# Kernel optimization log

Hardware: AMD Instinct MI355X
Metric: run time of the kernel (lower is better)

Reference implementation:

```python
import jax, jax.numpy as jnp
import numpy as np

NEG_SLOPE = 0.2

def _l2norm(x):
    # F.normalize(x, 2, -1): x / max(||x||_2, 1e-12)
    return x / jnp.maximum(jnp.linalg.norm(x, axis=-1, keepdims=True), 1e-12)

def _segment_softmax(e, dst, n_dst):
    m = jax.ops.segment_max(e, dst, num_segments=n_dst)
    m = jnp.where(jnp.isfinite(m), m, 0.0)
    ex = jnp.exp(e - m[dst])
    denom = jax.ops.segment_sum(ex, dst, num_segments=n_dst)
    return ex / (denom[dst] + 1e-16)

def _gat_conv(x_src, x_dst, edge_index, W, a_src, a_dst, b, n_dst):
    # PyG GATConv, heads=1, concat, shared lin for src/dst (int in_channels)
    h_src = x_src @ W                      # [Ns, H]
    h_dst = x_dst @ W                      # [Nd, H]
    src, dst = edge_index[0], edge_index[1]
    al_s = h_src @ a_src                   # [Ns]
    al_d = h_dst @ a_dst                   # [Nd]
    e = jax.nn.leaky_relu(al_s[src] + al_d[dst], NEG_SLOPE)  # [E]
    coef = _segment_softmax(e, dst, n_dst)                   # [E]
    out = jax.ops.segment_sum(coef[:, None] * h_src[src], dst, num_segments=n_dst)
    return out + b

def setup_inputs() -> dict:
    key = jax.random.key(0)
    ks = jax.random.split(key, 32)
    nd, npr, nc, H, L, B = 2000, 19000, 100, 256, 2, 8192
    E_pp, E_dp, E_cp = 400000, 60000, 300000
    s = 0.1
    inp = {
        'drug_emb': jax.random.normal(ks[0], (nd, H), jnp.float32),
        'protein_emb': jax.random.normal(ks[1], (npr, H), jnp.float32),
        'cell_emb': jax.random.normal(ks[2], (nc, H), jnp.float32),
        'W_pp': jax.random.normal(ks[3], (L, H, H), jnp.float32) * s,
        'as_pp': jax.random.normal(ks[4], (L, H), jnp.float32) * s,
        'ad_pp': jax.random.normal(ks[5], (L, H), jnp.float32) * s,
        'b_pp': jax.random.normal(ks[6], (L, H), jnp.float32) * s,
        'W_dp': jax.random.normal(ks[7], (L, H, H), jnp.float32) * s,
        'as_dp': jax.random.normal(ks[8], (L, H), jnp.float32) * s,
        'ad_dp': jax.random.normal(ks[9], (L, H), jnp.float32) * s,
        'b_dp': jax.random.normal(ks[10], (L, H), jnp.float32) * s,
        'W_cp': jax.random.normal(ks[11], (L, H, H), jnp.float32) * s,
        'as_cp': jax.random.normal(ks[12], (L, H), jnp.float32) * s,
        'ad_cp': jax.random.normal(ks[13], (L, H), jnp.float32) * s,
        'b_cp': jax.random.normal(ks[14], (L, H), jnp.float32) * s,
        'W1': jax.random.normal(ks[15], (3 * H, 6 * H), jnp.float32) * s,
        'b1': jax.random.normal(ks[16], (6 * H,), jnp.float32) * s,
        'W2': jax.random.normal(ks[17], (6 * H, 2 * H), jnp.float32) * s,
        'b2': jax.random.normal(ks[18], (2 * H,), jnp.float32) * s,
        'W3': jax.random.normal(ks[19], (2 * H, 2), jnp.float32) * s,
        'b3': jax.random.normal(ks[20], (2,), jnp.float32) * s,
        'edge_pp': jnp.stack([jax.random.randint(ks[21], (E_pp,), 0, npr),
                              jax.random.randint(ks[22], (E_pp,), 0, npr)]),
        'edge_dp': jnp.stack([jax.random.randint(ks[23], (E_dp,), 0, npr),
                              jax.random.randint(ks[24], (E_dp,), 0, nd)]),
        'edge_cp': jnp.stack([jax.random.randint(ks[25], (E_cp,), 0, npr),
                              jax.random.randint(ks[26], (E_cp,), 0, nc)]),
        'drug1': jax.random.randint(ks[27], (B,), 0, nd),
        'drug2': jax.random.randint(ks[28], (B,), 0, nd),
        'cell': jax.random.randint(ks[29], (B,), 0, nc),
    }
    return inp

def reference(drug_emb, protein_emb, cell_emb,
              W_pp, as_pp, ad_pp, b_pp,
              W_dp, as_dp, ad_dp, b_dp,
              W_cp, as_cp, ad_cp, b_cp,
              W1, b1, W2, b2, W3, b3,
              edge_pp, edge_dp, edge_cp, drug1, drug2, cell):
    n_drug, n_prot, n_cell = drug_emb.shape[0], protein_emb.shape[0], cell_emb.shape[0]
    num_layer = W_pp.shape[0]
    # node ids are arange -> embedding lookup is the full table
    x_d, x_p, x_c = drug_emb, protein_emb, cell_emb
    # p-p GATConv adds self loops (default add_self_loops=True)
    loop = jnp.arange(n_prot, dtype=edge_pp.dtype)
    ei_pp = jnp.concatenate([edge_pp, jnp.stack([loop, loop])], axis=1)
    for l in range(num_layer):
        x_p = _gat_conv(x_p, x_p, ei_pp, W_pp[l], as_pp[l], ad_pp[l], b_pp[l], n_prot)
        x_p = _l2norm(x_p)
        x_d = jax.nn.relu(_gat_conv(x_p, x_d, edge_dp, W_dp[l], as_dp[l], ad_dp[l], b_dp[l], n_drug))
        x_c = jax.nn.relu(_gat_conv(x_p, x_c, edge_cp, W_cp[l], as_cp[l], ad_cp[l], b_cp[l], n_cell))
    hid = jnp.concatenate([_l2norm(x_d[drug1]), _l2norm(x_d[drug2]), _l2norm(x_c[cell])], axis=1)
    h = jax.nn.relu(hid @ W1 + b1)
    h = jax.nn.relu(h @ W2 + b2)
    logits = h @ W3 + b3
    return logits
```

## Files before the change

kernel.cpp:

```cpp
#include <hip/hip_runtime.h>
#include <hip/hip_bf16.h>

#define HDIM 256
#define NEG_SLOPE 0.2f
#define NB 128
#define SLICES 8
#define TBN 64
#define TBK 32

typedef __attribute__((ext_vector_type(8))) short bf16x8;
typedef __attribute__((ext_vector_type(4))) float f32x4;

__device__ inline uint f2pl(float x) {
  __hip_bfloat16 h = __float2bfloat16(x);
  ushort hi = *(ushort*)&h;
  float r = x - __bfloat162float(h);
  __hip_bfloat16 l = __float2bfloat16(r);
  ushort lo = *(ushort*)&l;
  return (uint)hi | ((uint)lo << 16);
}
__device__ inline ushort f2b(float x) {
  __hip_bfloat16 h = __float2bfloat16(x);
  return *(ushort*)&h;
}
__device__ inline float b2f(ushort u) {
  uint x = ((uint)u) << 16;
  return __int_as_float((int)x);
}

static inline int cdiv(int a, int b) { return (a + b - 1) / b; }

__global__ void fillf_kernel(float* __restrict__ p, float v, int n) {
  int i = blockIdx.x * blockDim.x + threadIdx.x;
  if (i < n) p[i] = v;
}

__global__ void fill_out2_kernel(float* __restrict__ out, const float* __restrict__ b3, int M) {
  int i = blockIdx.x * 256 + threadIdx.x;
  if (i >= M) return;
  out[(size_t)i * 2 + 0] = b3[0];
  out[(size_t)i * 2 + 1] = b3[1];
}

__global__ void wconv_split_kernel(const float* __restrict__ W,
                                   ushort* __restrict__ WTh, ushort* __restrict__ WTl,
                                   int K, int N) {
  int i = blockIdx.x * 256 + threadIdx.x;
  if (i >= K * N) return;
  int k = i / N, n = i - k * N;
  uint p = f2pl(W[i]);
  WTh[(size_t)n * K + k] = (ushort)(p & 0xffff);
  WTl[(size_t)n * K + k] = (ushort)(p >> 16);
}

__global__ void wconv_split3_kernel(
    const float* __restrict__ Wpp, const float* __restrict__ Wdp, const float* __restrict__ Wcp,
    ushort* __restrict__ WTpph, ushort* __restrict__ WTppl,
    ushort* __restrict__ WTdph, ushort* __restrict__ WTdpl,
    ushort* __restrict__ WTcph, ushort* __restrict__ WTcpl, int L) {
  const int per = HDIM * HDIM;
  int i = blockIdx.x * 256 + threadIdx.x;
  if (i >= 3 * L * per) return;
  int mat = i / per;
  int r = i - mat * per;
  int l = mat / 3, ty = mat - l * 3;
  const float* W = (ty == 0 ? Wpp : ty == 1 ? Wdp : Wcp) + (size_t)l * per;
  ushort* Th = (ty == 0 ? WTpph : ty == 1 ? WTdph : WTcph) + (size_t)l * per;
  ushort* Tl = (ty == 0 ? WTppl : ty == 1 ? WTdpl : WTcpl) + (size_t)l * per;
  int k = r >> 8, n = r & (HDIM - 1);
  uint p = f2pl(W[r]);
  Th[(size_t)n * HDIM + k] = (ushort)(p & 0xffff);
  Tl[(size_t)n * HDIM + k] = (ushort)(p >> 16);
}

__global__ void f32_to_split_kernel(const float* __restrict__ in,
                                    ushort* __restrict__ oh, ushort* __restrict__ ol, int n) {
  int i = blockIdx.x * 256 + threadIdx.x;
  if (i >= n) return;
  uint p = f2pl(in[i]);
  oh[i] = (ushort)(p & 0xffff);
  ol[i] = (ushort)(p >> 16);
}

__global__ __launch_bounds__(256) void matvec_all_kernel(
    const float* __restrict__ Wpp, const float* __restrict__ aspp, const float* __restrict__ adpp,
    const float* __restrict__ Wdp, const float* __restrict__ asdp, const float* __restrict__ addp,
    const float* __restrict__ Wcp, const float* __restrict__ ascp, const float* __restrict__ adcp,
    float* __restrict__ wv) {
  int b = blockIdx.x;
  int l = b / 6, r = b - l * 6, type = r >> 1, isd = r & 1;
  const float* W = (type == 0 ? Wpp : type == 1 ? Wdp : Wcp) + (size_t)l * HDIM * HDIM;
  const float* a = (type == 0 ? (isd ? adpp : aspp)
                  : type == 1 ? (isd ? addp : asdp)
                              : (isd ? adcp : ascp)) + (size_t)l * HDIM;
  int k = threadIdx.x;
  const float4* Wr = (const float4*)(W + (size_t)k * HDIM);
  float s = 0.f;
#pragma unroll 8
  for (int n4 = 0; n4 < HDIM / 4; ++n4) {
    float4 w = Wr[n4];
    float4 av = *(const float4*)(a + n4 * 4);
    s += w.x * av.x + w.y * av.y + w.z * av.z + w.w * av.w;
  }
  wv[(size_t)b * HDIM + k] = s;
}

__global__ __launch_bounds__(256) void prep_p_kernel(
    const float* __restrict__ in, ushort* __restrict__ outb,
    const float* __restrict__ a1, const float* __restrict__ a2,
    float* __restrict__ o1, float* __restrict__ o2, int n) {
  int row = blockIdx.x * 4 + (threadIdx.x >> 6);
  if (row >= n) return;
  int lane = threadIdx.x & 63;
  float s1 = 0.f, s2 = 0.f;
#pragma unroll
  for (int u = 0; u < 4; ++u) {
    int c = lane + u * 64;
    float hv = in[(size_t)row * HDIM + c];
    outb[(size_t)row * HDIM + c] = f2b(hv);
    s1 += hv * a1[c];
    s2 += hv * a2[c];
  }
#pragma unroll
  for (int off = 32; off; off >>= 1) {
    s1 += __shfl_down(s1, off);
    s2 += __shfl_down(s2, off);
  }
  if (lane == 0) { o1[row] = s1; o2[row] = s2; }
}

__global__ __launch_bounds__(256) void combine_h1_kernel(
    const float* __restrict__ P1, const float* __restrict__ P2, const float* __restrict__ P3,
    const int* __restrict__ g1, const int* __restrict__ g2, const int* __restrict__ g3,
    int row0, ushort* __restrict__ h1h, ushort* __restrict__ h1l, int M, int K) {
  int t = blockIdx.x * 256 + threadIdx.x;
  int kq = K >> 2;
  if (t >= M * kq) return;
  int row = t / kq, c4 = t - row * kq;
  int bi = row0 + row;
  size_t o = (size_t)c4 * 4;
  float4 a = *(const float4*)(P1 + (size_t)g1[bi] * K + o);
  float4 b = *(const float4*)(P2 + (size_t)g2[bi] * K + o);
  float4 c = *(const float4*)(P3 + (size_t)g3[bi] * K + o);
  uint p0 = f2pl(fmaxf(a.x + b.x + c.x, 0.f));
  uint p1 = f2pl(fmaxf(a.y + b.y + c.y, 0.f));
  uint p2 = f2pl(fmaxf(a.z + b.z + c.z, 0.f));
  uint p3 = f2pl(fmaxf(a.w + b.w + c.w, 0.f));
  ushort4 h = {(ushort)(p0 & 0xffff), (ushort)(p1 & 0xffff), (ushort)(p2 & 0xffff), (ushort)(p3 & 0xffff)};
  ushort4 l = {(ushort)(p0 >> 16), (ushort)(p1 >> 16), (ushort)(p2 >> 16), (ushort)(p3 >> 16)};
  *(ushort4*)(h1h + (size_t)row * K + o) = h;
  *(ushort4*)(h1l + (size_t)row * K + o) = l;
}

template <int TBM_, int ACT, int FUSE3>
__global__ __launch_bounds__(256) void mfma_gemm(
    const ushort* __restrict__ Ahg, const ushort* __restrict__ Alg,
    const ushort* __restrict__ Bhg, const ushort* __restrict__ Blg,
    int ldb, const float* __restrict__ bias, const float* __restrict__ W3g,
    float* __restrict__ C, int M, int N, int K) {
  __shared__ __align__(16) ushort Ah[2][4][TBM_ / 16][16][8];
  __shared__ __align__(16) ushort Al[2][4][TBM_ / 16][16][8];
  __shared__ __align__(16) ushort Bh[2][4][TBN / 16][16][8];
  __shared__ __align__(16) ushort Bl[2][4][TBN / 16][16][8];

  constexpr int NU = TBM_ / 64;
  constexpr int TM = TBM_ / 32;

  const int tid = threadIdx.x;
  const int lane = tid & 63;
  const int wid = tid >> 6;
  const int wm = wid & 1, wn = wid >> 1;
  const int l16 = lane & 15;
  const int quad = lane >> 4;
  const int m0 = blockIdx.x * TBM_;
  const int n0 = blockIdx.y * TBN;

  const int gq = lane & 3;
  const int co = gq * 8;
  const int r4 = lane >> 2;
  const int wslot = (r4 + 2 * gq) & 15;
  const int rslot = (l16 + 2 * quad) & 15;

  uint4 rah0[NU], ral0[NU], rbh0, rbl0;
  uint4 rah1[NU], ral1[NU], rbh1, rbl1;

  auto LOADA = [&](uint4* rah, uint4* ral, uint4& rbh, uint4& rbl, int k0) {
#pragma unroll
    for (int u = 0; u < NU; ++u) {
      int r = wid * (TBM_ / 4) + r4 + 16 * u;
      int gm = m0 + r;
      if (gm < M) {
        size_t o = (size_t)gm * K + k0 + co;
        rah[u] = *(const uint4*)(Ahg + o);
        ral[u] = *(const uint4*)(Alg + o);
      } else {
        rah[u] = make_uint4(0, 0, 0, 0);
        ral[u] = make_uint4(0, 0, 0, 0);
      }
    }
    {
      int r = wid * 16 + r4;
      size_t o = (size_t)(n0 + r) * ldb + k0 + co;
      rbh = *(const uint4*)(Bhg + o);
      rbl = *(const uint4*)(Blg + o);
    }
  };
  auto STORE = [&](const uint4* rah, const uint4* ral, const uint4& rbh, const uint4& rbl, int b) {
#pragma unroll
    for (int u = 0; u < NU; ++u) {
      int ch = (wid * (TBM_ / 4) + 16 * u) >> 4;
      *(uint4*)&Ah[b][gq][ch][wslot][0] = rah[u];
      *(uint4*)&Al[b][gq][ch][wslot][0] = ral[u];
    }
    *(uint4*)&Bh[b][gq][wid][wslot][0] = rbh;
    *(uint4*)&Bl[b][gq][wid][wslot][0] = rbl;
  };

  f32x4 acc[TM][2];
#pragma unroll
  for (int i = 0; i < TM; ++i)
#pragma unroll
    for (int j = 0; j < 2; ++j) acc[i][j] = (f32x4){0.f, 0.f, 0.f, 0.f};

  auto COMPUTE = [&](int b) {
    bf16x8 ahf[TM], alf[TM], bhf[2], blf[2];
#pragma unroll
    for (int t = 0; t < TM; ++t) {
      int ch = wm * (TBM_ / 32) + t;
      ahf[t] = *(const bf16x8*)&Ah[b][quad][ch][rslot][0];
      alf[t] = *(const bf16x8*)&Al[b][quad][ch][rslot][0];
    }
#pragma unroll
    for (int t = 0; t < 2; ++t) {
      int ch = wn * 2 + t;
      bhf[t] = *(const bf16x8*)&Bh[b][quad][ch][rslot][0];
      blf[t] = *(const bf16x8*)&Bl[b][quad][ch][rslot][0];
    }
#pragma unroll
    for (int tm = 0; tm < TM; ++tm)
#pragma unroll
      for (int tn = 0; tn < 2; ++tn) {
        acc[tm][tn] = __builtin_amdgcn_mfma_f32_16x16x32_bf16(ahf[tm], bhf[tn], acc[tm][tn], 0, 0, 0);
        acc[tm][tn] = __builtin_amdgcn_mfma_f32_16x16x32_bf16(ahf[tm], blf[tn], acc[tm][tn], 0, 0, 0);
        acc[tm][tn] = __builtin_amdgcn_mfma_f32_16x16x32_bf16(alf[tm], bhf[tn], acc[tm][tn], 0, 0, 0);
      }
  };

  const int NK = K / TBK;
  LOADA(rah0, ral0, rbh0, rbl0, 0);
  LOADA(rah1, ral1, rbh1, rbl1, TBK);
  STORE(rah0, ral0, rbh0, rbl0, 0);
  int k = 2 * TBK;
  for (int t = 0; t < (NK - 2) / 2; ++t) {
    __syncthreads();
    LOADA(rah0, ral0, rbh0, rbl0, k);
    COMPUTE(0);
    STORE(rah1, ral1, rbh1, rbl1, 1);
    k += TBK;
    __syncthreads();
    LOADA(rah1, ral1, rbh1, rbl1, k);
    COMPUTE(1);
    STORE(rah0, ral0, rbh0, rbl0, 0);
    k += TBK;
  }
  __syncthreads();
  COMPUTE(0);
  STORE(rah1, ral1, rbh1, rbl1, 1);
  __syncthreads();
  COMPUTE(1);

  if (FUSE3) {
#pragma unroll
    for (int tm = 0; tm < TM; ++tm) {
#pragma unroll
      for (int r = 0; r < 4; ++r) {
        int row = m0 + wm * (TBM_ / 2) + tm * 16 + quad * 4 + r;
        float s0 = 0.f, s1 = 0.f;
#pragma unroll
        for (int tn = 0; tn < 2; ++tn) {
          int col = n0 + wn * 32 + tn * 16 + l16;
          float v = fmaxf(acc[tm][tn][r] + bias[col], 0.f);
          s0 += v * W3g[col * 2 + 0];
          s1 += v * W3g[col * 2 + 1];
        }
#pragma unroll
        for (int o = 1; o < 16; o <<= 1) {
          s0 += __shfl_xor(s0, o);
          s1 += __shfl_xor(s1, o);
        }
        if (l16 == 0 && row < M) {
          atomicAdd(&C[(size_t)row * 2 + 0], s0);
          atomicAdd(&C[(size_t)row * 2 + 1], s1);
        }
      }
    }
  } else {
#pragma unroll
    for (int tn = 0; tn < 2; ++tn) {
      int col = n0 + wn * 32 + tn * 16 + l16;
      float bv = bias ? bias[col] : 0.f;
#pragma unroll
      for (int tm = 0; tm < TM; ++tm) {
#pragma unroll
        for (int r = 0; r < 4; ++r) {
          int row = m0 + wm * (TBM_ / 2) + tm * 16 + quad * 4 + r;
          if (row >= M) continue;
          float v = acc[tm][tn][r] + bv;
          if (ACT == 1) v = fmaxf(v, 0.f);
          C[(size_t)row * N + col] = v;
        }
      }
    }
  }
}

template <int TBM_, int ACT>
static void gemm_launch(hipStream_t s,
                        const ushort* Ahg, const ushort* Alg,
                        const ushort* Bhg, const ushort* Blg,
                        int ldb, const float* bias, float* C,
                        int M, int N, int K) {
  dim3 g(cdiv(M, TBM_), N / TBN);
  mfma_gemm<TBM_, ACT, 0><<<g, 256, 0, s>>>(Ahg, Alg, Bhg, Blg, ldb, bias, nullptr, C, M, N, K);
}

static void gemm_launch_f3(hipStream_t s,
                           const ushort* Ahg, const ushort* Alg,
                           const ushort* Bhg, const ushort* Blg,
                           int ldb, const float* bias, const float* W3,
                           float* C, int M, int N, int K) {
  dim3 g(cdiv(M, 64), N / TBN);
  mfma_gemm<64, 1, 1><<<g, 256, 0, s>>>(Ahg, Alg, Bhg, Blg, ldb, bias, W3, C, M, N, K);
}

__global__ __launch_bounds__(256) void rowdot_kernel(
    const float* __restrict__ H, const float* __restrict__ a,
    float* __restrict__ out, int n) {
  int row = blockIdx.x * 4 + (threadIdx.x >> 6);
  if (row >= n) return;
  int lane = threadIdx.x & 63;
  const float* h = H + (size_t)row * HDIM;
  float s = 0.f;
#pragma unroll
  for (int u = 0; u < 4; ++u) {
    int c = lane + u * 64;
    s += h[c] * a[c];
  }
#pragma unroll
  for (int off = 32; off; off >>= 1) s += __shfl_down(s, off);
  if (lane == 0) out[row] = s;
}

__global__ __launch_bounds__(256) void hist_kernel(
    const int* __restrict__ src, const int* __restrict__ dst, int E, int nloops,
    int Nd, int* __restrict__ offs) {
  extern __shared__ int bins[];
  int tot = E + nloops;
  int chunk = (tot + NB - 1) / NB;
  int b = blockIdx.x;
  int s0 = b * chunk, s1 = min(s0 + chunk, tot);
  for (int i = threadIdx.x; i < Nd; i += 256) bins[i] = 0;
  __syncthreads();
  for (int i = s0 + threadIdx.x; i < s1; i += 256) {
    int d = (i < E) ? dst[i] : (i - E);
    atomicAdd(&bins[d], 1);
  }
  __syncthreads();
  for (int i = threadIdx.x; i < Nd; i += 256) offs[(size_t)i * NB + b] = bins[i];
}

__global__ __launch_bounds__(256) void scan_bins_kernel(
    int* __restrict__ offs, int* __restrict__ binsum, int Nd) {
  int d = blockIdx.x * 4 + (threadIdx.x >> 6);
  if (d >= Nd) return;
  int lane = threadIdx.x & 63;
  int* p = offs + (size_t)d * NB;
  int v0 = p[2 * lane], v1 = p[2 * lane + 1];
  int s = v0 + v1;
  int t = s;
#pragma unroll
  for (int o = 1; o < 64; o <<= 1) { int u = __shfl_up(t, o); if (lane >= o) t += u; }
  int excl = t - s;
  p[2 * lane] = excl;
  p[2 * lane + 1] = excl + v0;
  if (lane == 63) binsum[d] = t;
}

__global__ __launch_bounds__(256) void scan_base_kernel(
    const int* __restrict__ binsum, int* __restrict__ rowptr, int Nd) {
  __shared__ int wsum[4];
  __shared__ int carry;
  if (threadIdx.x == 0) carry = 0;
  __syncthreads();
  int lane = threadIdx.x & 63, w = threadIdx.x >> 6;
  for (int t0 = 0; t0 < Nd; t0 += 256) {
    int i = t0 + threadIdx.x;
    int v = (i < Nd) ? binsum[i] : 0;
    int t = v;
#pragma unroll
    for (int o = 1; o < 64; o <<= 1) { int u = __shfl_up(t, o); if (lane >= o) t += u; }
    if (lane == 63) wsum[w] = t;
    __syncthreads();
    int add = carry;
    for (int k = 0; k < w; ++k) add += wsum[k];
    if (i < Nd) rowptr[i] = t - v + add;
    __syncthreads();
    if (threadIdx.x == 0) carry += wsum[0] + wsum[1] + wsum[2] + wsum[3];
    __syncthreads();
  }
  if (threadIdx.x == 0) rowptr[Nd] = carry;
}

__global__ __launch_bounds__(256) void scatter_kernel(
    const int* __restrict__ src, const int* __restrict__ dst, int E, int nloops,
    int Nd, const int* __restrict__ offs, const int* __restrict__ rowptr,
    uint* __restrict__ sd) {
  extern __shared__ int bins[];
  int tot = E + nloops;
  int chunk = (tot + NB - 1) / NB;
  int b = blockIdx.x;
  int s0 = b * chunk, s1 = min(s0 + chunk, tot);
  for (int i = threadIdx.x; i < Nd; i += 256) bins[i] = 0;
  __syncthreads();
  for (int i = s0 + threadIdx.x; i < s1; i += 256) {
    int s_, d_;
    if (i < E) { s_ = src[i]; d_ = dst[i]; }
    else       { s_ = d_ = i - E; }
    int local = atomicAdd(&bins[d_], 1);
    int pos = rowptr[d_] + offs[(size_t)d_ * NB + b] + local;
    sd[pos] = (uint)s_ | ((uint)d_ << 16);
  }
}

__global__ __launch_bounds__(256) void gat_agg_split(
    const int* __restrict__ rowptr, const uint* __restrict__ sd,
    const float* __restrict__ als, const float* __restrict__ ald,
    const ushort* __restrict__ Xb,
    ushort* __restrict__ aggh, ushort* __restrict__ aggl, int n) {
  int d = blockIdx.x * 4 + (threadIdx.x >> 6);
  if (d >= n) return;
  int lane = threadIdx.x & 63;
  int r0 = rowptr[d], r1 = rowptr[d + 1];
  float aldd = ald[d];
  float dsum = 0.f;
  for (int j = r0 + lane; j < r1; j += 64) {
    float e = als[sd[j] & 0xffff] + aldd;
    e = (e > 0.f) ? e : NEG_SLOPE * e;
    dsum += __expf(e);
  }
#pragma unroll
  for (int o = 32; o; o >>= 1) dsum += __shfl_xor(dsum, o);
  float rden = 1.f / (dsum + 1e-16f);

  float4 acc = make_float4(0.f, 0.f, 0.f, 0.f);
  for (int b = r0; b < r1; b += 64) {
    int j = b + lane;
    float exv = 0.f; int srcv = 0;
    if (j < r1) {
      uint p = sd[j];
      srcv = p & 0xffff;
      float e = als[srcv] + aldd;
      e = (e > 0.f) ? e : NEG_SLOPE * e;
      exv = __expf(e) * rden;
    }
    int cnt = min(64, r1 - b);
    for (int t0 = 0; t0 < cnt; t0 += 8) {
      float cf[8]; int sv[8];
#pragma unroll
      for (int u = 0; u < 8; ++u) {
        cf[u] = __shfl(exv, t0 + u);
        sv[u] = __shfl(srcv, t0 + u);
      }
      ushort4 hv[8];
#pragma unroll
      for (int u = 0; u < 8; ++u)
        hv[u] = *(const ushort4*)(Xb + (size_t)sv[u] * HDIM + lane * 4);
#pragma unroll
      for (int u = 0; u < 8; ++u) {
        acc.x += cf[u] * b2f(hv[u].x);
        acc.y += cf[u] * b2f(hv[u].y);
        acc.z += cf[u] * b2f(hv[u].z);
        acc.w += cf[u] * b2f(hv[u].w);
      }
    }
  }
  uint p0 = f2pl(acc.x), p1 = f2pl(acc.y), p2 = f2pl(acc.z), p3 = f2pl(acc.w);
  ushort4 h = {(ushort)(p0 & 0xffff), (ushort)(p1 & 0xffff), (ushort)(p2 & 0xffff), (ushort)(p3 & 0xffff)};
  ushort4 l = {(ushort)(p0 >> 16), (ushort)(p1 >> 16), (ushort)(p2 >> 16), (ushort)(p3 >> 16)};
  *(ushort4*)(aggh + (size_t)d * HDIM + lane * 4) = h;
  *(ushort4*)(aggl + (size_t)d * HDIM + lane * 4) = l;
}

__global__ __launch_bounds__(256) void gat_agg_slice(
    const int* __restrict__ rowptr, const uint* __restrict__ sd,
    const float* __restrict__ als, const float* __restrict__ ald,
    const ushort* __restrict__ Xb, float* __restrict__ out32, int n) {
  int d = blockIdx.x / SLICES;
  int sl = blockIdx.x - d * SLICES;
  if (d >= n) return;
  int lane = threadIdx.x & 63, w = threadIdx.x >> 6;
  int r0 = rowptr[d], r1 = rowptr[d + 1];
  float aldd = ald[d];
  float dsum = 0.f;
  for (int j = r0 + threadIdx.x; j < r1; j += 256) {
    float e = als[sd[j] & 0xffff] + aldd;
    e = (e > 0.f) ? e : NEG_SLOPE * e;
    dsum += __expf(e);
  }
#pragma unroll
  for (int o = 32; o; o >>= 1) dsum += __shfl_xor(dsum, o);
  __shared__ float wd[4];
  if (lane == 0) wd[w] = dsum;
  __syncthreads();
  float rden = 1.f / (wd[0] + wd[1] + wd[2] + wd[3] + 1e-16f);
  int deg = r1 - r0;
  int per_b = (deg + SLICES - 1) / SLICES;
  int b0 = r0 + sl * per_b, b1 = min(b0 + per_b, r1);
  int wdeg = b1 - b0;
  if (wdeg <= 0) return;
  int per_w = (wdeg + 3) >> 2;
  int w0 = b0 + w * per_w, w1 = min(w0 + per_w, b1);

  float4 acc = make_float4(0.f, 0.f, 0.f, 0.f);
  for (int b = w0; b < w1; b += 64) {
    int j = b + lane;
    float exv = 0.f; int srcv = 0;
    if (j < w1) {
      uint p = sd[j];
      srcv = p & 0xffff;
      float e = als[srcv] + aldd;
      e = (e > 0.f) ? e : NEG_SLOPE * e;
      exv = __expf(e) * rden;
    }
    int cnt = min(64, w1 - b);
    for (int t0 = 0; t0 < cnt; t0 += 8) {
      float cf[8]; int sv[8];
#pragma unroll
      for (int u = 0; u < 8; ++u) {
        cf[u] = __shfl(exv, t0 + u);
        sv[u] = __shfl(srcv, t0 + u);
      }
      ushort4 hv[8];
#pragma unroll
      for (int u = 0; u < 8; ++u)
        hv[u] = *(const ushort4*)(Xb + (size_t)sv[u] * HDIM + lane * 4);
#pragma unroll
      for (int u = 0; u < 8; ++u) {
        acc.x += cf[u] * b2f(hv[u].x);
        acc.y += cf[u] * b2f(hv[u].y);
        acc.z += cf[u] * b2f(hv[u].z);
        acc.w += cf[u] * b2f(hv[u].w);
      }
    }
  }
  float* o = out32 + (size_t)d * HDIM + lane * 4;
  atomicAdd(o + 0, acc.x); atomicAdd(o + 1, acc.y);
  atomicAdd(o + 2, acc.z); atomicAdd(o + 3, acc.w);
}

__global__ __launch_bounds__(256) void l2norm_f32b_dots_kernel(
    const float* __restrict__ in, float* __restrict__ outf, ushort* __restrict__ outb,
    const float* __restrict__ v1, const float* __restrict__ v2,
    const float* __restrict__ v3, const float* __restrict__ v4,
    float* __restrict__ o1, float* __restrict__ o2,
    float* __restrict__ o3, float* __restrict__ o4, int n) {
  int row = blockIdx.x * 4 + (threadIdx.x >> 6);
  if (row >= n) return;
  int lane = threadIdx.x & 63;
  float v[4];
  float ss = 0.f;
#pragma unroll
  for (int u = 0; u < 4; ++u) {
    float t = in[(size_t)row * HDIM + lane + u * 64];
    v[u] = t; ss += t * t;
  }
#pragma unroll
  for (int off = 32; off; off >>= 1) ss += __shfl_xor(ss, off);
  float sc = 1.0f / fmaxf(sqrtf(ss), 1e-12f);
  float d1 = 0.f, d2 = 0.f, d3 = 0.f, d4 = 0.f;
#pragma unroll
  for (int u = 0; u < 4; ++u) {
    float f = v[u] * sc;
    int c = lane + u * 64;
    outf[(size_t)row * HDIM + c] = f;
    outb[(size_t)row * HDIM + c] = f2b(f);
    d1 += f * v1[c];
    d2 += f * v2[c];
    if (o3) { d3 += f * v3[c]; d4 += f * v4[c]; }
  }
#pragma unroll
  for (int off = 32; off; off >>= 1) {
    d1 += __shfl_xor(d1, off);
    d2 += __shfl_xor(d2, off);
    if (o3) { d3 += __shfl_xor(d3, off); d4 += __shfl_xor(d4, off); }
  }
  if (lane == 0) {
    o1[row] = d1; o2[row] = d2;
    if (o3) { o3[row] = d3; o4[row] = d4; }
  }
}

__global__ __launch_bounds__(256) void l2norm_split_kernel(
    const float* __restrict__ in,
    ushort* __restrict__ oh, ushort* __restrict__ ol, int n) {
  int row = blockIdx.x * 4 + (threadIdx.x >> 6);
  if (row >= n) return;
  int lane = threadIdx.x & 63;
  float v[4];
  float ss = 0.f;
#pragma unroll
  for (int u = 0; u < 4; ++u) {
    int c = lane + u * 64;
    float t = in[(size_t)row * HDIM + c];
    v[u] = t;
    ss += t * t;
  }
#pragma unroll
  for (int off = 32; off; off >>= 1) ss += __shfl_xor(ss, off);
  float sc = 1.0f / fmaxf(sqrtf(ss), 1e-12f);
#pragma unroll
  for (int u = 0; u < 4; ++u) {
    int c = lane + u * 64;
    uint p = f2pl(v[u] * sc);
    oh[(size_t)row * HDIM + c] = (ushort)(p & 0xffff);
    ol[(size_t)row * HDIM + c] = (ushort)(p >> 16);
  }
}

static void build_sorted(hipStream_t stream,
                         const int* src, const int* dst, int E, int nloops, int Nd,
                         int* offs, int* binsum, int* rowptr, uint* sd) {
  size_t lds = (size_t)Nd * sizeof(int);
  hist_kernel<<<NB, 256, lds, stream>>>(src, dst, E, nloops, Nd, offs);
  scan_bins_kernel<<<cdiv(Nd, 4), 256, 0, stream>>>(offs, binsum, Nd);
  scan_base_kernel<<<1, 256, 0, stream>>>(binsum, rowptr, Nd);
  scatter_kernel<<<NB, 256, lds, stream>>>(src, dst, E, nloops, Nd, offs, rowptr, sd);
}

extern "C" void kernel_launch(void* const* d_in, const int* in_sizes, int n_in,
                              void* d_out, int out_size, void* d_ws, size_t ws_size,
                              hipStream_t stream) {
  const float* drug_emb = (const float*)d_in[0];
  const float* prot_emb = (const float*)d_in[1];
  const float* cell_emb = (const float*)d_in[2];
  const float* W_pp = (const float*)d_in[3];
  const float* as_pp = (const float*)d_in[4];
  const float* ad_pp = (const float*)d_in[5];
  const float* b_pp = (const float*)d_in[6];
  const float* W_dp = (const float*)d_in[7];
  const float* as_dp = (const float*)d_in[8];
  const float* ad_dp = (const float*)d_in[9];
  const float* b_dp = (const float*)d_in[10];
  const float* W_cp = (const float*)d_in[11];
  const float* as_cp = (const float*)d_in[12];
  const float* ad_cp = (const float*)d_in[13];
  const float* b_cp = (const float*)d_in[14];
  const float* W1 = (const float*)d_in[15];
  const float* b1 = (const float*)d_in[16];
  const float* W2 = (const float*)d_in[17];
  const float* b2 = (const float*)d_in[18];
  const float* W3 = (const float*)d_in[19];
  const float* b3 = (const float*)d_in[20];
  const int* edge_pp = (const int*)d_in[21];
  const int* edge_dp = (const int*)d_in[22];
  const int* edge_cp = (const int*)d_in[23];
  const int* drug1 = (const int*)d_in[24];
  const int* drug2 = (const int*)d_in[25];
  const int* cellb = (const int*)d_in[26];

  const int ND = in_sizes[0] / HDIM;
  const int NP = in_sizes[1] / HDIM;
  const int NC = in_sizes[2] / HDIM;
  const int L = in_sizes[3] / (HDIM * HDIM);
  const int E_pp = in_sizes[21] / 2;
  const int E_dp = in_sizes[22] / 2;
  const int E_cp = in_sizes[23] / 2;
  const int B = in_sizes[24];
  (void)n_in; (void)out_size;

  const int* src_pp = edge_pp;          const int* dst_pp = edge_pp + E_pp;
  const int* src_dp = edge_dp;          const int* dst_dp = edge_dp + E_dp;
  const int* src_cp = edge_cp;          const int* dst_cp = edge_cp + E_cp;
  const int tot_pp = E_pp + NP, tot_dp = E_dp, tot_cp = E_cp;
  int maxN = NP > ND ? NP : ND; if (NC > maxN) maxN = NC;

  char* wsb = (char*)d_ws;
  size_t off = 0;
  auto alloc = [&](size_t bytes) -> void* {
    void* p = wsb + off;
    off += (bytes + 255) & ~(size_t)255;
    return p;
  };

  float* Xp  = (float*)alloc((size_t)NP * HDIM * 4);
  ushort* Xpb = (ushort*)alloc((size_t)NP * HDIM * 2);
  float* Xd  = (float*)alloc((size_t)ND * HDIM * 4);
  float* Xc  = (float*)alloc((size_t)NC * HDIM * 4);
  ushort* xdnh = (ushort*)alloc((size_t)ND * HDIM * 2);
  ushort* xdnl = (ushort*)alloc((size_t)ND * HDIM * 2);
  ushort* xcnh = (ushort*)alloc((size_t)NC * HDIM * 2);
  ushort* xcnl = (ushort*)alloc((size_t)NC * HDIM * 2);
  ushort* WTpph = (ushort*)alloc((size_t)L * HDIM * HDIM * 2);
  ushort* WTppl = (ushort*)alloc((size_t)L * HDIM * HDIM * 2);
  ushort* WTdph = (ushort*)alloc((size_t)L * HDIM * HDIM * 2);
  ushort* WTdpl = (ushort*)alloc((size_t)L * HDIM * HDIM * 2);
  ushort* WTcph = (ushort*)alloc((size_t)L * HDIM * HDIM * 2);
  ushort* WTcpl = (ushort*)alloc((size_t)L * HDIM * HDIM * 2);
  ushort* cth = (ushort*)alloc((size_t)NC * HDIM * 2);
  ushort* ctl = (ushort*)alloc((size_t)NC * HDIM * 2);
  float* wv  = (float*)alloc((size_t)L * 6 * HDIM * 4);
  float* pals = (float*)alloc((size_t)maxN * 4);
  float* pald = (float*)alloc((size_t)maxN * 4);
  float* als1 = (float*)alloc((size_t)maxN * 4);
  float* als2 = (float*)alloc((size_t)maxN * 4);
  float* ald1 = (float*)alloc((size_t)maxN * 4);
  float* ald2 = (float*)alloc((size_t)maxN * 4);
  int* binsum = (int*)alloc((size_t)maxN * 4);
  int* rp_pp = (int*)alloc((size_t)(NP + 1) * 4);
  int* rp_dp = (int*)alloc((size_t)(ND + 1) * 4);
  int* rp_cp = (int*)alloc((size_t)(NC + 1) * 4);
  uint* sd_pp = (uint*)alloc((size_t)tot_pp * 4);
  uint* sd_dp = (uint*)alloc((size_t)tot_dp * 4);
  uint* sd_cp = (uint*)alloc((size_t)tot_cp * 4);
  float* out32 = (float*)alloc((size_t)NC * HDIM * 4);
  size_t S0 = off;

  int* offs = (int*)(wsb + S0);
  build_sorted(stream, src_pp, dst_pp, E_pp, NP, NP, offs, binsum, rp_pp, sd_pp);
  build_sorted(stream, src_dp, dst_dp, E_dp, 0, ND, offs, binsum, rp_dp, sd_dp);
  build_sorted(stream, src_cp, dst_cp, E_cp, 0, NC, offs, binsum, rp_cp, sd_cp);

  wconv_split3_kernel<<<cdiv(3 * L * HDIM * HDIM, 256), 256, 0, stream>>>(
      W_pp, W_dp, W_cp, WTpph, WTppl, WTdph, WTdpl, WTcph, WTcpl, L);
  matvec_all_kernel<<<L * 6, 256, 0, stream>>>(W_pp, as_pp, ad_pp, W_dp, as_dp, ad_dp,
                                               W_cp, as_cp, ad_cp, wv);
  prep_p_kernel<<<cdiv(NP, 4), 256, 0, stream>>>(prot_emb, Xpb, wv + 0 * HDIM, wv + 1 * HDIM,
                                                 pals, pald, NP);

  size_t aggB = ((size_t)NP * HDIM * 2 + 255) & ~(size_t)255;
  ushort* aggh = (ushort*)(wsb + S0);
  ushort* aggl = (ushort*)(wsb + S0 + aggB);
  float* tmp = (float*)(wsb + S0 + 2 * aggB);

  for (int l = 0; l < L; ++l) {
    const int WOFF = l * HDIM * HDIM, VOFF = l * HDIM;
    const float* wvl = wv + (size_t)l * 6 * HDIM;
    bool last = (l == L - 1);
    const float* wvn = last ? wvl : wv + (size_t)(l + 1) * 6 * HDIM;
    const float* Xd_cur = (l == 0) ? drug_emb : Xd;
    const float* Xc_cur = (l == 0) ? cell_emb : Xc;

    gat_agg_split<<<cdiv(NP, 4), 256, 0, stream>>>(rp_pp, sd_pp, pals, pald, Xpb, aggh, aggl, NP);
    gemm_launch<128, 0>(stream, aggh, aggl, WTpph + WOFF, WTppl + WOFF, HDIM,
                        b_pp + VOFF, tmp, NP, HDIM, HDIM);
    l2norm_f32b_dots_kernel<<<cdiv(NP, 4), 256, 0, stream>>>(
        tmp, Xp, Xpb,
        wvl + 2 * HDIM, wvl + 4 * HDIM,
        last ? nullptr : (wvn + 0 * HDIM), last ? nullptr : (wvn + 1 * HDIM),
        als1, als2, last ? nullptr : pals, last ? nullptr : pald, NP);

    rowdot_kernel<<<cdiv(ND, 4), 256, 0, stream>>>(Xd_cur, wvl + 3 * HDIM, ald1, ND);
    rowdot_kernel<<<cdiv(NC, 4), 256, 0, stream>>>(Xc_cur, wvl + 5 * HDIM, ald2, NC);

    gat_agg_split<<<cdiv(ND, 4), 256, 0, stream>>>(rp_dp, sd_dp, als1, ald1, Xpb, aggh, aggl, ND);
    gemm_launch<64, 1>(stream, aggh, aggl, WTdph + WOFF, WTdpl + WOFF, HDIM,
                       b_dp + VOFF, Xd, ND, HDIM, HDIM);

    fillf_kernel<<<cdiv(NC * HDIM, 256), 256, 0, stream>>>(out32, 0.f, NC * HDIM);
    gat_agg_slice<<<NC * SLICES, 256, 0, stream>>>(rp_cp, sd_cp, als2, ald2, Xpb, out32, NC);
    f32_to_split_kernel<<<cdiv(NC * HDIM, 256), 256, 0, stream>>>(out32, cth, ctl, NC * HDIM);
    gemm_launch<64, 1>(stream, cth, ctl, WTcph + WOFF, WTcpl + WOFF, HDIM,
                       b_cp + VOFF, Xc, NC, HDIM, HDIM);
  }

  l2norm_split_kernel<<<cdiv(ND, 4), 256, 0, stream>>>(Xd, xdnh, xdnl, ND);
  l2norm_split_kernel<<<cdiv(NC, 4), 256, 0, stream>>>(Xc, xcnh, xcnl, NC);

  const int N1 = 6 * HDIM;
  const int N2 = 2 * HDIM;
  const int K1 = 3 * HDIM;
  ushort* W1Th = (ushort*)(wsb + S0);
  ushort* W1Tl = W1Th + (size_t)N1 * K1;
  ushort* W2Th = W1Tl + (size_t)N1 * K1;
  ushort* W2Tl = W2Th + (size_t)N2 * N1;
  float* P1 = (float*)(W2Tl + (size_t)N2 * N1);
  float* P2 = P1 + (size_t)ND * N1;
  float* P3 = P2 + (size_t)ND * N1;
  ushort* h1h = (ushort*)(P3 + (size_t)NC * N1);
  size_t wsz = ws_size ? ws_size : ((size_t)1 << 30);
  size_t fixed = S0 + ((size_t)N1 * K1 + (size_t)N2 * N1) * 4
               + ((size_t)(2 * ND + NC) * N1) * 4;
  int CH = 8192;
  while (CH > 1024 && fixed + (size_t)CH * N1 * 4 > wsz) CH >>= 1;
  ushort* h1l = h1h + (size_t)CH * N1;

  wconv_split_kernel<<<cdiv(K1 * N1, 256), 256, 0, stream>>>(W1, W1Th, W1Tl, K1, N1);
  wconv_split_kernel<<<cdiv(N1 * N2, 256), 256, 0, stream>>>(W2, W2Th, W2Tl, N1, N2);

  gemm_launch<64, 0>(stream, xdnh, xdnl, W1Th, W1Tl, K1, nullptr, P1, ND, N1, HDIM);
  gemm_launch<64, 0>(stream, xdnh, xdnl, W1Th + HDIM, W1Tl + HDIM, K1, nullptr, P2, ND, N1, HDIM);
  gemm_launch<64, 0>(stream, xcnh, xcnl, W1Th + 2 * HDIM, W1Tl + 2 * HDIM, K1, b1, P3, NC, N1, HDIM);

  float* outp = (float*)d_out;
  fill_out2_kernel<<<cdiv(B, 256), 256, 0, stream>>>(outp, b3, B);
  for (int c0 = 0; c0 < B; c0 += CH) {
    int M = (B - c0) < CH ? (B - c0) : CH;
    combine_h1_kernel<<<cdiv(M * (N1 / 4), 256), 256, 0, stream>>>(
        P1, P2, P3, drug1, drug2, cellb, c0, h1h, h1l, M, N1);
    gemm_launch_f3(stream, h1h, h1l, W2Th, W2Tl, N1, b2, W3,
                   outp + (size_t)c0 * 2, M, N2, N1);
  }
}
```

Baseline: 707.6 us.

## Load GEMM B fragments directly from global into registers, drop B LDS staging

```diff
diff --git a/kernel.cpp b/kernel.cpp
--- a/kernel.cpp
+++ b/kernel.cpp
@@ -160,8 +160,6 @@
     float* __restrict__ C, int M, int N, int K) {
   __shared__ __align__(16) ushort Ah[2][4][TBM_ / 16][16][8];
   __shared__ __align__(16) ushort Al[2][4][TBM_ / 16][16][8];
-  __shared__ __align__(16) ushort Bh[2][4][TBN / 16][16][8];
-  __shared__ __align__(16) ushort Bl[2][4][TBN / 16][16][8];
 
   constexpr int NU = TBM_ / 64;
   constexpr int TM = TBM_ / 32;
@@ -181,10 +179,17 @@
   const int wslot = (r4 + 2 * gq) & 15;
   const int rslot = (l16 + 2 * quad) & 15;
 
-  uint4 rah0[NU], ral0[NU], rbh0, rbl0;
-  uint4 rah1[NU], ral1[NU], rbh1, rbl1;
-
-  auto LOADA = [&](uint4* rah, uint4* ral, uint4& rbh, uint4& rbl, int k0) {
+  size_t boff[2];
+#pragma unroll
+  for (int t = 0; t < 2; ++t)
+    boff[t] = (size_t)(n0 + wn * 32 + t * 16 + l16) * ldb + quad * 8;
+
+  uint4 rah0[NU], ral0[NU];
+  uint4 rah1[NU], ral1[NU];
+  bf16x8 fbh0[2], fbl0[2];
+  bf16x8 fbh1[2], fbl1[2];
+
+  auto LOADA = [&](uint4* rah, uint4* ral, int k0) {
 #pragma unroll
     for (int u = 0; u < NU; ++u) {
       int r = wid * (TBM_ / 4) + r4 + 16 * u;
@@ -198,22 +203,21 @@
         ral[u] = make_uint4(0, 0, 0, 0);
       }
     }
-    {
-      int r = wid * 16 + r4;
-      size_t o = (size_t)(n0 + r) * ldb + k0 + co;
-      rbh = *(const uint4*)(Bhg + o);
-      rbl = *(const uint4*)(Blg + o);
-    }
   };
-  auto STORE = [&](const uint4* rah, const uint4* ral, const uint4& rbh, const uint4& rbl, int b) {
+  auto LOADB = [&](bf16x8* bh, bf16x8* bl, int k0) {
+#pragma unroll
+    for (int t = 0; t < 2; ++t) {
+      bh[t] = *(const bf16x8*)(Bhg + boff[t] + k0);
+      bl[t] = *(const bf16x8*)(Blg + boff[t] + k0);
+    }
+  };
+  auto STORE = [&](const uint4* rah, const uint4* ral, int b) {
 #pragma unroll
     for (int u = 0; u < NU; ++u) {
       int ch = (wid * (TBM_ / 4) + 16 * u) >> 4;
       *(uint4*)&Ah[b][gq][ch][wslot][0] = rah[u];
       *(uint4*)&Al[b][gq][ch][wslot][0] = ral[u];
     }
-    *(uint4*)&Bh[b][gq][wid][wslot][0] = rbh;
-    *(uint4*)&Bl[b][gq][wid][wslot][0] = rbl;
   };
 
   f32x4 acc[TM][2];
@@ -222,19 +226,13 @@
 #pragma unroll
     for (int j = 0; j < 2; ++j) acc[i][j] = (f32x4){0.f, 0.f, 0.f, 0.f};
 
-  auto COMPUTE = [&](int b) {
-    bf16x8 ahf[TM], alf[TM], bhf[2], blf[2];
+  auto COMPUTE = [&](int b, const bf16x8* bhf, const bf16x8* blf) {
+    bf16x8 ahf[TM], alf[TM];
 #pragma unroll
     for (int t = 0; t < TM; ++t) {
       int ch = wm * (TBM_ / 32) + t;
       ahf[t] = *(const bf16x8*)&Ah[b][quad][ch][rslot][0];
       alf[t] = *(const bf16x8*)&Al[b][quad][ch][rslot][0];
-    }
-#pragma unroll
-    for (int t = 0; t < 2; ++t) {
-      int ch = wn * 2 + t;
-      bhf[t] = *(const bf16x8*)&Bh[b][quad][ch][rslot][0];
-      blf[t] = *(const bf16x8*)&Bl[b][quad][ch][rslot][0];
     }
 #pragma unroll
     for (int tm = 0; tm < TM; ++tm)
@@ -247,27 +245,31 @@
   };
 
   const int NK = K / TBK;
-  LOADA(rah0, ral0, rbh0, rbl0, 0);
-  LOADA(rah1, ral1, rbh1, rbl1, TBK);
-  STORE(rah0, ral0, rbh0, rbl0, 0);
+  LOADA(rah0, ral0, 0);
+  LOADA(rah1, ral1, TBK);
+  STORE(rah0, ral0, 0);
+  LOADB(fbh0, fbl0, 0);
   int k = 2 * TBK;
   for (int t = 0; t < (NK - 2) / 2; ++t) {
     __syncthreads();
-    LOADA(rah0, ral0, rbh0, rbl0, k);
-    COMPUTE(0);
-    STORE(rah1, ral1, rbh1, rbl1, 1);
+    LOADA(rah0, ral0, k);
+    LOADB(fbh1, fbl1, k - TBK);
+    COMPUTE(0, fbh0, fbl0);
+    STORE(rah1, ral1, 1);
     k += TBK;
     __syncthreads();
-    LOADA(rah1, ral1, rbh1, rbl1, k);
-    COMPUTE(1);
-    STORE(rah0, ral0, rbh0, rbl0, 0);
+    LOADA(rah1, ral1, k);
+    LOADB(fbh0, fbl0, k - TBK);
+    COMPUTE(1, fbh1, fbl1);
+    STORE(rah0, ral0, 0);
     k += TBK;
   }
   __syncthreads();
-  COMPUTE(0);
-  STORE(rah1, ral1, rbh1, rbl1, 1);
+  LOADB(fbh1, fbl1, (NK - 1) * TBK);
+  COMPUTE(0, fbh0, fbl0);
+  STORE(rah1, ral1, 1);
   __syncthreads();
-  COMPUTE(1);
+  COMPUTE(1, fbh1, fbl1);
 
   if (FUSE3) {
 #pragma unroll
@@ -329,8 +331,8 @@
                            const ushort* Bhg, const ushort* Blg,
                            int ldb, const float* bias, const float* W3,
                            float* C, int M, int N, int K) {
-  dim3 g(cdiv(M, 64), N / TBN);
-  mfma_gemm<64, 1, 1><<<g, 256, 0, s>>>(Ahg, Alg, Bhg, Blg, ldb, bias, W3, C, M, N, K);
+  dim3 g(cdiv(M, 128), N / TBN);
+  mfma_gemm<128, 1, 1><<<g, 256, 0, s>>>(Ahg, Alg, Bhg, Blg, ldb, bias, W3, C, M, N, K);
 }
 
 __global__ __launch_bounds__(256) void rowdot_kernel(
```

Measured after the change: 739.6 us. 1.05x slower.
